# Kernel tuning notes

Hardware: AMD Instinct MI355X
Metric: run time of the kernel (lower is better)

The kernel has to match this reference:

```python
import jax, jax.numpy as jnp
import numpy as np

B, N, K = 2, 8192, 16
D_IN, D_OUT = 32, 128
EPS = 1e-5


def _bn(x, gamma, beta):
    # x: (B, C, L); BatchNorm1d training-mode stats over (B, L)
    mean = x.mean(axis=(0, 2), keepdims=True)
    var = x.var(axis=(0, 2), keepdims=True)
    return gamma[None, :, None] * (x - mean) * jax.lax.rsqrt(var + EPS) + beta[None, :, None]


def _shared_mlp(x, w, b, gamma, beta, act):
    # SharedMLP: 1x1 Conv1d (channel GEMM) + BN + activation. x: (B, Cin, L)
    y = jnp.einsum('oi,bil->bol', w, x) + b[None, :, None]
    return act(_bn(y, gamma, beta))


def _attentive_pool(x, w, b):
    # x: (B, C, N, K); per-(b,n,k) Linear over C, softmax over K, weighted sum over K
    scores = jnp.einsum('oc,bcnk->bonk', w, x) + b[None, :, None, None]
    scores = jax.nn.softmax(scores, axis=-1)
    return jnp.sum(scores * x, axis=-1)  # (B, C, N)  (torch keeps K=1 dim; squeezed by SharedMLP reshape)


def _knn(coords, k):
    # brute-force squared-L2 KNN excluding self (faiss IndexFlatL2 semantics)
    sq = jnp.sum(coords * coords, axis=-1)  # (B, N)
    d2 = sq[:, :, None] + sq[:, None, :] - 2.0 * jnp.einsum('bid,bjd->bij', coords, coords)
    n = coords.shape[1]
    d2 = jnp.where(jnp.eye(n, dtype=bool)[None], jnp.inf, d2)
    neg, idx = jax.lax.top_k(-d2, k)  # ascending squared distance
    return idx, jnp.maximum(-neg, 0.0)


def _lse(coords, features, idx, dist, w, b, gamma, beta):
    # LocalSpatialEncoding: gather neighbor coords, build 10-ch relative features, MLP, concat
    Bq, Nq, Kq = idx.shape
    neighbor = jax.vmap(lambda c, i: c[i])(coords, idx)  # (B, N, K, 3)
    center = jnp.broadcast_to(coords[:, :, None, :], neighbor.shape)
    rel = center - neighbor
    spatial = jnp.concatenate([center, neighbor, rel, dist[..., None]], axis=-1)  # (B, N, K, 10)
    spatial = spatial.transpose(0, 3, 1, 2).reshape(Bq, 10, Nq * Kq)
    sf = _shared_mlp(spatial, w, b, gamma, beta, jax.nn.relu).reshape(Bq, -1, Nq, Kq)
    feat = jnp.broadcast_to(features[..., None], (Bq, features.shape[1], Nq, Kq))
    return jnp.concatenate([sf, feat], axis=1)


def _forward(coords, features,
             mlp1_w, mlp1_b, mlp1_g, mlp1_bt,
             lse1_w, lse1_b, lse1_g, lse1_bt,
             mlpp1_w, mlpp1_b, mlpp1_g, mlpp1_bt,
             lse2_w, lse2_b, lse2_g, lse2_bt,
             mlp2_w, mlp2_b, mlp2_g, mlp2_bt,
             res_w, res_b, res_g, res_bt,
             pool1_w, pool1_b, pool2_w, pool2_b):
    # faiss output is detached in torch (numpy round-trip) -> stop_gradient
    idx, dist = _knn(jax.lax.stop_gradient(coords), K)
    lrelu02 = lambda v: jnp.where(v >= 0, v, 0.2 * v)   # LeakyReLU(0.2)
    lrelu01 = lambda v: jnp.where(v >= 0, v, 0.01 * v)  # default LeakyReLU
    x = _shared_mlp(features, mlp1_w, mlp1_b, mlp1_g, mlp1_bt, lrelu02)      # (B, 64, N)
    x = _lse(coords, x, idx, dist, lse1_w, lse1_b, lse1_g, lse1_bt)          # (B, 128, N, K)
    x = _attentive_pool(x, pool1_w, pool1_b)                                  # (B, 128, N)
    x = _shared_mlp(x, mlpp1_w, mlpp1_b, mlpp1_g, mlpp1_bt, jax.nn.relu)     # (B, 32, N)
    x = _lse(coords, x, idx, dist, lse2_w, lse2_b, lse2_g, lse2_bt)          # (B, 64, N, K)
    x = _attentive_pool(x, pool2_w, pool2_b)                                  # (B, 64, N)
    x_main = _shared_mlp(x, mlp2_w, mlp2_b, mlp2_g, mlp2_bt, jax.nn.relu)    # (B, 128, N)
    resid = _shared_mlp(features, res_w, res_b, res_g, res_bt, jax.nn.relu)  # (B, 128, N)
    return lrelu01(jnp.concatenate([x_main, resid], axis=1))                 # (B, 256, N)


def setup_inputs() -> dict:
    key = jax.random.key(0)
    ks = iter(jax.random.split(key, 64))

    def lin(ci, co):
        w = jax.random.normal(next(ks), (co, ci), jnp.float32) / np.float32(np.sqrt(ci))
        b = jax.random.normal(next(ks), (co,), jnp.float32) * 0.01
        return w, b

    inp = {}
    inp['coords'] = jax.random.normal(next(ks), (B, N, 3), jnp.float32)
    inp['features'] = jax.random.normal(next(ks), (B, D_IN, N), jnp.float32)
    for name, ci, co in [('mlp1', D_IN, D_OUT // 2), ('lse1', 10, D_OUT // 2),
                         ('mlpp1', D_OUT, D_OUT // 4), ('lse2', 10, D_OUT // 4),
                         ('mlp2', D_OUT // 2, D_OUT), ('res', D_IN, D_OUT)]:
        w, b = lin(ci, co)
        inp[name + '_w'], inp[name + '_b'] = w, b
        inp[name + '_g'] = jnp.ones((co,), jnp.float32)
        inp[name + '_bt'] = jnp.zeros((co,), jnp.float32)
    for name, c in [('pool1', D_OUT), ('pool2', D_OUT // 2)]:
        w, b = lin(c, c)
        inp[name + '_w'], inp[name + '_b'] = w, b
    return inp


def reference(coords, features,
              mlp1_w, mlp1_b, mlp1_g, mlp1_bt,
              lse1_w, lse1_b, lse1_g, lse1_bt,
              mlpp1_w, mlpp1_b, mlpp1_g, mlpp1_bt,
              lse2_w, lse2_b, lse2_g, lse2_bt,
              mlp2_w, mlp2_b, mlp2_g, mlp2_bt,
              res_w, res_b, res_g, res_bt,
              pool1_w, pool1_b, pool2_w, pool2_b):
    return _forward(coords, features,
                    mlp1_w, mlp1_b, mlp1_g, mlp1_bt,
                    lse1_w, lse1_b, lse1_g, lse1_bt,
                    mlpp1_w, mlpp1_b, mlpp1_g, mlpp1_bt,
                    lse2_w, lse2_b, lse2_g, lse2_bt,
                    mlp2_w, mlp2_b, mlp2_g, mlp2_bt,
                    res_w, res_b, res_g, res_bt,
                    pool1_w, pool1_b, pool2_w, pool2_b)
```

## Files before the change

kernel.cpp:

```cpp
#include <hip/hip_runtime.h>

static constexpr int N_ = 8192;
static constexpr int B_ = 2;
static constexpr int K_ = 16;

typedef __attribute__((ext_vector_type(8))) short bf16x8;
typedef __attribute__((ext_vector_type(4))) float f32x4;

__device__ __forceinline__ short f2bf(float f) {
  unsigned int u = __float_as_uint(f);
  unsigned int r = (u + 0x7FFFu + ((u >> 16) & 1u)) >> 16;
  return (short)r;
}
__device__ __forceinline__ float bf2f(short h) {
  return __uint_as_float(((unsigned int)(unsigned short)h) << 16);
}
__device__ __forceinline__ float dpp_shr1_f(float x) {
  return __uint_as_float((unsigned int)__builtin_amdgcn_update_dpp(
      0, (int)__float_as_uint(x), 0x111, 0xF, 0xF, true));
}
__device__ __forceinline__ int dpp_shr1_i(int x) {
  return __builtin_amdgcn_update_dpp(0, x, 0x111, 0xF, 0xF, true);
}
__device__ __forceinline__ float rdlane_f(float x, int l) {
  return __uint_as_float(__builtin_amdgcn_readlane(__float_as_uint(x), l));
}

__global__ __launch_bounds__(512) void knn_kernel(const float* __restrict__ coords,
                                                  int* __restrict__ oidx,
                                                  float* __restrict__ odist) {
  __shared__ float4 pts[2048];
  const int b = blockIdx.y;
  const int wv = threadIdx.x >> 6;
  const int lane = threadIdx.x & 63;
  const bool lpos = (lane != 0);
  const int q0 = blockIdx.x * 16 + wv * 2;
  const int q1 = q0 + 1;
  const float* cb = coords + (size_t)b * N_ * 3;
  const float qx0 = cb[q0 * 3 + 0], qy0 = cb[q0 * 3 + 1], qz0 = cb[q0 * 3 + 2];
  const float qx1 = cb[q1 * 3 + 0], qy1 = cb[q1 * 3 + 1], qz1 = cb[q1 * 3 + 2];
  const float qsq0 = fmaf(qx0, qx0, fmaf(qy0, qy0, qz0 * qz0));
  const float qsq1 = fmaf(qx1, qx1, fmaf(qy1, qy1, qz1 * qz1));
  const int qblk0 = q0 & ~63, qblk1 = q1 & ~63;
  const unsigned long long qbit0 = ~(1ull << (q0 & 63));
  const unsigned long long qbit1 = ~(1ull << (q1 & 63));
  float kd0 = INFINITY, kd1 = INFINITY;
  int ki0 = 0, ki1 = 0;
  float tau0 = INFINITY, tau1 = INFINITY;
  for (int t0 = 0; t0 < N_; t0 += 2048) {
    __syncthreads();
    for (int i = threadIdx.x; i < 2048; i += 512) {
      const int p = t0 + i;
      const float x = cb[p * 3 + 0], y = cb[p * 3 + 1], z = cb[p * 3 + 2];
      const float sq = fmaf(x, x, fmaf(y, y, z * z));
      pts[i] = make_float4(x, y, z, sq);
    }
    __syncthreads();
    for (int s = 0; s < 2048; s += 64) {
      const float4 p = pts[s + lane];
      const int base = t0 + s;
      const float dot0 = fmaf(qx0, p.x, fmaf(qy0, p.y, qz0 * p.z));
      const float dot1 = fmaf(qx1, p.x, fmaf(qy1, p.y, qz1 * p.z));
      const float d20 = fmaf(-2.0f, dot0, qsq0 + p.w);
      const float d21 = fmaf(-2.0f, dot1, qsq1 + p.w);
      unsigned long long m0 = __ballot(d20 < tau0);
      unsigned long long m1 = __ballot(d21 < tau1);
      if (base == qblk0) m0 &= qbit0;
      if (base == qblk1) m1 &= qbit1;
      if (m0) {
        do {
          const int src = __builtin_ctzll(m0);
          const float dc = rdlane_f(d20, src);
          const int jc = base + src;
          const float sd = dpp_shr1_f(kd0);
          const int si = dpp_shr1_i(ki0);
          const bool c1 = kd0 > dc;
          const bool c2 = lpos && (sd > dc);
          kd0 = c1 ? (c2 ? sd : dc) : kd0;
          ki0 = c1 ? (c2 ? si : jc) : ki0;
          m0 &= (m0 - 1);
        } while (m0);
        tau0 = rdlane_f(kd0, 15);
      }
      if (m1) {
        do {
          const int src = __builtin_ctzll(m1);
          const float dc = rdlane_f(d21, src);
          const int jc = base + src;
          const float sd = dpp_shr1_f(kd1);
          const int si = dpp_shr1_i(ki1);
          const bool c1 = kd1 > dc;
          const bool c2 = lpos && (sd > dc);
          kd1 = c1 ? (c2 ? sd : dc) : kd1;
          ki1 = c1 ? (c2 ? si : jc) : ki1;
          m1 &= (m1 - 1);
        } while (m1);
        tau1 = rdlane_f(kd1, 15);
      }
    }
  }
  if (lane < 16) {
    oidx[((size_t)b * N_ + q0) * K_ + lane] = ki0;
    odist[((size_t)b * N_ + q0) * K_ + lane] = fmaxf(kd0, 0.0f);
    oidx[((size_t)b * N_ + q1) * K_ + lane] = ki1;
    odist[((size_t)b * N_ + q1) * K_ + lane] = fmaxf(kd1, 0.0f);
  }
}

__device__ __forceinline__ float snn_get(const float* SNN, int a, int b) {
  const int i = a < b ? a : b, j = a < b ? b : a;
  return SNN[i == 0 ? j : (i == 1 ? 2 + j : 3 + j)];
}
__device__ __forceinline__ float mom_mean(int i, const float* C, const float* SN, float Sd) {
  if (i < 3) return 16.0f * C[i];
  if (i < 6) return SN[i - 3];
  if (i < 9) return 16.0f * C[i - 6] - SN[i - 6];
  return Sd;
}
__device__ __forceinline__ float mom_prod(int i, int j, const float* C, const float* SN,
                                          const float* SNN, float Sd, float Sdd, const float* SND) {
  const int ti = i < 3 ? 0 : (i < 6 ? 1 : (i < 9 ? 2 : 3));
  const int tj = j < 3 ? 0 : (j < 6 ? 1 : (j < 9 ? 2 : 3));
  const int a = (ti == 3) ? 0 : (i - ti * 3);
  const int bb = (tj == 3) ? 0 : (j - tj * 3);
  if (ti == 0 && tj == 0) return 16.0f * C[a] * C[bb];
  if (ti == 0 && tj == 1) return C[a] * SN[bb];
  if (ti == 0 && tj == 2) return C[a] * (16.0f * C[bb] - SN[bb]);
  if (ti == 0 && tj == 3) return C[a] * Sd;
  if (ti == 1 && tj == 1) return snn_get(SNN, a, bb);
  if (ti == 1 && tj == 2) return C[bb] * SN[a] - snn_get(SNN, a, bb);
  if (ti == 1 && tj == 3) return SND[a];
  if (ti == 2 && tj == 2) return 16.0f * C[a] * C[bb] - C[a] * SN[bb] - C[bb] * SN[a] + snn_get(SNN, a, bb);
  if (ti == 2 && tj == 3) return C[a] * Sd - SND[a];
  return Sdd;
}

__global__ __launch_bounds__(64) void moments_kernel(const float* __restrict__ coords,
                                                     const int* __restrict__ knn_i,
                                                     const float* __restrict__ knn_d,
                                                     double* __restrict__ mom) {
  const int t = blockIdx.x * 64 + threadIdx.x;
  const int b = t >> 13, n = t & (N_ - 1);
  const float* cb = coords + (size_t)b * N_ * 3;
  float C[3] = {cb[n * 3 + 0], cb[n * 3 + 1], cb[n * 3 + 2]};
  float SN[3] = {0.f, 0.f, 0.f}, SNN[6] = {0.f, 0.f, 0.f, 0.f, 0.f, 0.f};
  float SND[3] = {0.f, 0.f, 0.f}, Sd = 0.f, Sdd = 0.f;
  for (int k = 0; k < K_; ++k) {
    const int id = knn_i[(size_t)t * K_ + k];
    const float dd = knn_d[(size_t)t * K_ + k];
    const float nx = cb[id * 3 + 0], ny = cb[id * 3 + 1], nz = cb[id * 3 + 2];
    SN[0] += nx; SN[1] += ny; SN[2] += nz;
    SNN[0] += nx * nx; SNN[1] += nx * ny; SNN[2] += nx * nz;
    SNN[3] += ny * ny; SNN[4] += ny * nz; SNN[5] += nz * nz;
    Sd += dd; Sdd += dd * dd;
    SND[0] += nx * dd; SND[1] += ny * dd; SND[2] += nz * dd;
  }
  float m65[65];
  int e = 0;
#pragma unroll
  for (int i = 0; i < 10; ++i) m65[e++] = mom_mean(i, C, SN, Sd);
#pragma unroll
  for (int i = 0; i < 10; ++i)
#pragma unroll
    for (int j = i; j < 10; ++j) m65[e++] = mom_prod(i, j, C, SN, SNN, Sd, Sdd, SND);
#pragma unroll
  for (int q = 0; q < 65; ++q) {
    float v = m65[q];
#pragma unroll
    for (int off = 32; off > 0; off >>= 1) v += __shfl_xor(v, off);
    m65[q] = v;
  }
  __shared__ float buf[65];
  if (threadIdx.x == 0) {
#pragma unroll
    for (int q = 0; q < 65; ++q) buf[q] = m65[q];
  }
  __syncthreads();
  if (threadIdx.x < 64) atomicAdd(&mom[threadIdx.x], (double)buf[threadIdx.x]);
  if (threadIdx.x == 0) atomicAdd(&mom[64], (double)buf[64]);
}

template <int CI, int CO>
__device__ __forceinline__ void conv_frag_seg(const float* __restrict__ w, short* __restrict__ H,
                                              short* __restrict__ L, int tid, int nthr) {
  constexpr int NT = CO / 16;
  for (int i = tid; i < CI * CO; i += nthr) {
    const int j = i & 7, l = (i >> 3) & 63, tmp = i >> 9;
    const int tt = tmp % NT, cc = tmp / NT;
    const int c = cc * 32 + (l >> 4) * 8 + j;
    const int o = tt * 16 + (l & 15);
    const float v = w[o * CI + c];
    const short h = f2bf(v);
    H[i] = h;
    L[i] = f2bf(v - bf2f(h));
  }
}

__global__ __launch_bounds__(256) void convert_kernel(
    const float* __restrict__ pw1, const float* __restrict__ pw2,
    short* __restrict__ wB1, short* __restrict__ wB2,
    const float* __restrict__ wm1, short* __restrict__ f1H, short* __restrict__ f1L,
    const float* __restrict__ wmp, short* __restrict__ f2H, short* __restrict__ f2L,
    const float* __restrict__ wm2, short* __restrict__ f3H, short* __restrict__ f3L,
    const float* __restrict__ wrs, short* __restrict__ fRH, short* __restrict__ fRL) {
  const int blk = blockIdx.x;
  if (blk < 8) {
    const int tid = blk * 256 + threadIdx.x;
    for (int i = tid; i < 128 * 128; i += 2048) wB1[i] = f2bf(pw1[i]);
  } else if (blk < 10) {
    const int tid = (blk - 8) * 256 + threadIdx.x;
    for (int i = tid; i < 64 * 64; i += 512) wB2[i] = f2bf(pw2[i]);
  } else if (blk < 12) {
    conv_frag_seg<32, 64>(wm1, f1H, f1L, (blk - 10) * 256 + threadIdx.x, 512);
  } else if (blk < 16) {
    conv_frag_seg<128, 32>(wmp, f2H, f2L, (blk - 12) * 256 + threadIdx.x, 1024);
  } else if (blk < 24) {
    conv_frag_seg<64, 128>(wm2, f3H, f3L, (blk - 16) * 256 + threadIdx.x, 2048);
  } else {
    conv_frag_seg<32, 128>(wrs, fRH, fRL, (blk - 24) * 256 + threadIdx.x, 1024);
  }
}

__global__ void setup_kernel(const double* __restrict__ mom,
                             const float* __restrict__ w1, const float* __restrict__ b1,
                             const float* __restrict__ g1, const float* __restrict__ t1,
                             const float* __restrict__ w2, const float* __restrict__ b2,
                             const float* __restrict__ g2, const float* __restrict__ t2,
                             float* __restrict__ w1f8, float* __restrict__ w2f8) {
  const int t = threadIdx.x;
  __shared__ double mu[10];
  __shared__ double S[10][10];
  const double cnt = (double)B_ * N_ * K_;
  if (t < 10) mu[t] = mom[t] / cnt;
  if (t < 55) {
    int e = t, i = 0;
    while (e >= 10 - i) { e -= 10 - i; ++i; }
    const int j = i + e;
    const double v = mom[10 + t] / cnt;
    S[i][j] = v;
    S[j][i] = v;
  }
  __syncthreads();
  const float *w, *bias, *gg, *bt;
  float *wf;
  int c;
  if (t < 64) { w = w1; bias = b1; gg = g1; bt = t1; wf = w1f8; c = t; }
  else if (t < 96) { w = w2; bias = b2; gg = g2; bt = t2; wf = w2f8; c = t - 64; }
  else return;
  double wd[10];
#pragma unroll
  for (int d = 0; d < 10; ++d) wd[d] = (double)w[c * 10 + d];
  const double cbv = (double)bias[c];
  double mz = cbv;
  for (int d = 0; d < 10; ++d) mz += wd[d] * mu[d];
  double e2 = cbv * cbv;
  for (int d = 0; d < 10; ++d) e2 += 2.0 * cbv * wd[d] * mu[d];
  for (int d = 0; d < 10; ++d)
    for (int e = 0; e < 10; ++e) e2 += wd[d] * wd[e] * S[d][e];
  const double var = e2 - mz * mz;
  const double a = (double)gg[c] / sqrt(var + 1e-5);
  const double shift = (double)bt[c] - a * mz;
  wf[c * 8 + 0] = (float)(a * (wd[0] + wd[6]));
  wf[c * 8 + 1] = (float)(a * (wd[1] + wd[7]));
  wf[c * 8 + 2] = (float)(a * (wd[2] + wd[8]));
  wf[c * 8 + 3] = (float)(a * (wd[3] - wd[6]));
  wf[c * 8 + 4] = (float)(a * (wd[4] - wd[7]));
  wf[c * 8 + 5] = (float)(a * (wd[5] - wd[8]));
  wf[c * 8 + 6] = (float)(a * wd[9]);
  wf[c * 8 + 7] = (float)(a * cbv + shift);
}

template <int CI, int CO, bool ROWMAJ>
__global__ __launch_bounds__(256) void gemm_mfma_kernel(const float* __restrict__ in,
                                                        const short* __restrict__ fragH,
                                                        const short* __restrict__ fragL,
                                                        const float* __restrict__ bias,
                                                        float* __restrict__ out,
                                                        double* __restrict__ sacc) {
  constexpr int NT = CO / 16;
  constexpr int NC = CI / 32;
  __shared__ float part[4][CO][2];
  const int wv = threadIdx.x >> 6, l = threadIdx.x & 63;
  const int col = l & 15, quad = l >> 4;
  const int p0 = blockIdx.x * 64 + wv * 16;
  const int pt = p0 + col;
  f32x4 d[NT];
#pragma unroll
  for (int t = 0; t < NT; ++t) {
    const float bv = bias[t * 16 + col];
    d[t][0] = bv; d[t][1] = bv; d[t][2] = bv; d[t][3] = bv;
  }
#pragma unroll
  for (int cc = 0; cc < NC; ++cc) {
    float xv[8];
    if (ROWMAJ) {
      const float* ip = in + (size_t)pt * CI + cc * 32 + quad * 8;
      *(float4*)&xv[0] = *(const float4*)ip;
      *(float4*)&xv[4] = *(const float4*)(ip + 4);
    } else {
      const int b = pt >> 13, n = pt & (N_ - 1);
      const float* ip = in + ((size_t)b * CI + cc * 32 + quad * 8) * N_ + n;
#pragma unroll
      for (int j = 0; j < 8; ++j) xv[j] = ip[(size_t)j * N_];
    }
    union { bf16x8 v; short u[8]; } AH, AL;
#pragma unroll
    for (int j = 0; j < 8; ++j) {
      const short h = f2bf(xv[j]);
      AH.u[j] = h;
      AL.u[j] = f2bf(xv[j] - bf2f(h));
    }
#pragma unroll
    for (int t = 0; t < NT; ++t) {
      const size_t fo = ((size_t)(cc * NT + t) * 64 + l) * 8;
      const bf16x8 BH = *(const bf16x8*)(fragH + fo);
      const bf16x8 BL = *(const bf16x8*)(fragL + fo);
      d[t] = __builtin_amdgcn_mfma_f32_16x16x32_bf16(AH.v, BH, d[t], 0, 0, 0);
      d[t] = __builtin_amdgcn_mfma_f32_16x16x32_bf16(AH.v, BL, d[t], 0, 0, 0);
      d[t] = __builtin_amdgcn_mfma_f32_16x16x32_bf16(AL.v, BH, d[t], 0, 0, 0);
    }
  }
#pragma unroll
  for (int t = 0; t < NT; ++t) {
#pragma unroll
    for (int r = 0; r < 4; ++r)
      out[(size_t)(p0 + quad * 4 + r) * CO + t * 16 + col] = d[t][r];
    float s1 = d[t][0] + d[t][1] + d[t][2] + d[t][3];
    float s2 = d[t][0] * d[t][0] + d[t][1] * d[t][1] + d[t][2] * d[t][2] + d[t][3] * d[t][3];
    s1 += __shfl_xor(s1, 16); s1 += __shfl_xor(s1, 32);
    s2 += __shfl_xor(s2, 16); s2 += __shfl_xor(s2, 32);
    if (quad == 0) { part[wv][t * 16 + col][0] = s1; part[wv][t * 16 + col][1] = s2; }
  }
  __syncthreads();
  if (threadIdx.x < CO) {
    const int o = threadIdx.x;
    atomicAdd(&sacc[o], (double)(part[0][o][0] + part[1][o][0] + part[2][o][0] + part[3][o][0]));
    atomicAdd(&sacc[CO + o], (double)(part[0][o][1] + part[1][o][1] + part[2][o][1] + part[3][o][1]));
  }
}

template <int CSF, int CF>
__global__ __launch_bounds__(256) void pool_kernel(
    const float* __restrict__ coords, const int* __restrict__ knn_i, const float* __restrict__ knn_d,
    const float* __restrict__ w8,
    const float* __restrict__ feat, const double* __restrict__ sfe,
    const float* __restrict__ gfe, const float* __restrict__ tfe,
    const float slope,
    const short* __restrict__ wB, const float* __restrict__ pb,
    float* __restrict__ out) {
  constexpr int C = CSF + CF;
  constexpr int CP = C + 4;
  constexpr int NT = C / 16;
  constexpr int NC = C / 32;
  __shared__ float xcat[4][16][CP];
  __shared__ float4 sp4[4][16];
  __shared__ float4 spc[4];
  const int g = threadIdx.x >> 6;
  const int l = threadIdx.x & 63;
  const int quad = l >> 4, col = l & 15;
  const int pid = blockIdx.x * 4 + g;
  const int b = pid >> 13, n = pid & (N_ - 1);
  const float* cb = coords + (size_t)b * N_ * 3;

  if (l < 16) {
    const int id = knn_i[(size_t)pid * K_ + l];
    const float dd = knn_d[(size_t)pid * K_ + l];
    const float nx = cb[id * 3 + 0], ny = cb[id * 3 + 1], nz = cb[id * 3 + 2];
    sp4[g][l] = make_float4(nx, ny, nz, dd);
    if (l == 0) spc[g] = make_float4(cb[n * 3 + 0], cb[n * 3 + 1], cb[n * 3 + 2], 0.0f);
  }
  if (l < CF) {
    const double cnt = (double)(B_ * N_);
    const double mean = sfe[l] / cnt;
    const double var = sfe[CF + l] / cnt - mean * mean;
    const double av = (double)gfe[l] / sqrt(var + 1e-5);
    const float af = (float)av;
    const float bfv = (float)((double)tfe[l] - av * mean);
    float v = feat[(size_t)pid * CF + l];
    v = af * v + bfv;
    v = (v >= 0.0f) ? v : slope * v;
#pragma unroll
    for (int j = 0; j < 16; ++j) xcat[g][j][CSF + l] = v;
  }
  __syncthreads();
  if (l < CSF) {
    const float4 wA = *(const float4*)(w8 + l * 8);
    const float4 wBv = *(const float4*)(w8 + l * 8 + 4);
    const float4 C4 = spc[g];
    const float tterm = wBv.w + wA.x * C4.x + wA.y * C4.y + wA.z * C4.z;
#pragma unroll
    for (int k = 0; k < 16; ++k) {
      const float4 nk = sp4[g][k];
      const float z = tterm + wA.w * nk.x + wBv.x * nk.y + wBv.y * nk.z + wBv.z * nk.w;
      xcat[g][k][l] = fmaxf(z, 0.0f);
    }
  }
  __syncthreads();
  f32x4 d[NT];
#pragma unroll
  for (int t = 0; t < NT; ++t) {
    const float pbv = pb[t * 16 + col];
    d[t][0] = pbv; d[t][1] = pbv; d[t][2] = pbv; d[t][3] = pbv;
  }
#pragma unroll
  for (int cc = 0; cc < NC; ++cc) {
    const float* xr = &xcat[g][col][cc * 32 + quad * 8];
    const float4 xa = *(const float4*)xr;
    const float4 xb = *(const float4*)(xr + 4);
    union { bf16x8 v; short u[8]; } A;
    A.u[0] = f2bf(xa.x); A.u[1] = f2bf(xa.y); A.u[2] = f2bf(xa.z); A.u[3] = f2bf(xa.w);
    A.u[4] = f2bf(xb.x); A.u[5] = f2bf(xb.y); A.u[6] = f2bf(xb.z); A.u[7] = f2bf(xb.w);
#pragma unroll
    for (int t = 0; t < NT; ++t) {
      const bf16x8 Bv = *(const bf16x8*)(wB + (size_t)(t * 16 + col) * C + cc * 32 + quad * 8);
      d[t] = __builtin_amdgcn_mfma_f32_16x16x32_bf16(A.v, Bv, d[t], 0, 0, 0);
    }
  }
#pragma unroll
  for (int t = 0; t < NT; ++t) {
    float mx = fmaxf(fmaxf(d[t][0], d[t][1]), fmaxf(d[t][2], d[t][3]));
    mx = fmaxf(mx, __shfl_xor(mx, 16));
    mx = fmaxf(mx, __shfl_xor(mx, 32));
    float e0 = __expf(d[t][0] - mx), e1 = __expf(d[t][1] - mx);
    float e2 = __expf(d[t][2] - mx), e3 = __expf(d[t][3] - mx);
    float s = e0 + e1 + e2 + e3;
    s += __shfl_xor(s, 16);
    s += __shfl_xor(s, 32);
    const int o = t * 16 + col;
    float part = e0 * xcat[g][quad * 4 + 0][o] + e1 * xcat[g][quad * 4 + 1][o] +
                 e2 * xcat[g][quad * 4 + 2][o] + e3 * xcat[g][quad * 4 + 3][o];
    part += __shfl_xor(part, 16);
    part += __shfl_xor(part, 32);
    if (quad == 0) out[(size_t)pid * C + o] = part / s;
  }
}

__global__ __launch_bounds__(256) void final_kernel(const float* __restrict__ y3,
                                                    const float* __restrict__ yr,
                                                    const double* __restrict__ s3,
                                                    const float* __restrict__ g3, const float* __restrict__ t3,
                                                    const double* __restrict__ sr,
                                                    const float* __restrict__ gr, const float* __restrict__ tr,
                                                    float* __restrict__ out) {
  __shared__ float tile[256 * 17];
  const int blk = blockIdx.x;
  const int b = blk >> 9;
  const int n0 = (blk & 511) << 4;
  const int c = threadIdx.x;
  const float* src;
  const double* sa;
  const float *gp, *tp;
  int cc;
  if (c < 128) { src = y3; sa = s3; gp = g3; tp = t3; cc = c; }
  else { src = yr; sa = sr; gp = gr; tp = tr; cc = c - 128; }
  const double cnt = (double)(B_ * N_);
  const double mean = sa[cc] / cnt;
  const double var = sa[128 + cc] / cnt - mean * mean;
  const double avd = (double)gp[cc] / sqrt(var + 1e-5);
  const float av = (float)avd;
  const float bv = (float)((double)tp[cc] - avd * mean);
#pragma unroll
  for (int nl = 0; nl < 16; ++nl) {
    const float x = av * src[((size_t)(b * N_ + n0 + nl)) * 128 + cc] + bv;
    tile[c * 17 + nl] = fmaxf(x, 0.0f);
  }
  __syncthreads();
  const int np = c & 15, grp = c >> 4;
#pragma unroll
  for (int j = 0; j < 16; ++j) {
    const int c2 = grp * 16 + j;
    out[((size_t)(b * 256 + c2)) * N_ + n0 + np] = tile[c2 * 17 + np];
  }
}

extern "C" void kernel_launch(void* const* d_in, const int* in_sizes, int n_in,
                              void* d_out, int out_size, void* d_ws, size_t ws_size,
                              hipStream_t stream) {
  (void)in_sizes; (void)n_in; (void)out_size; (void)ws_size;
  const float* coords   = (const float*)d_in[0];
  const float* features = (const float*)d_in[1];
  const float* mlp1_w = (const float*)d_in[2];
  const float* mlp1_b = (const float*)d_in[3];
  const float* mlp1_g = (const float*)d_in[4];
  const float* mlp1_t = (const float*)d_in[5];
  const float* lse1_w = (const float*)d_in[6];
  const float* lse1_b = (const float*)d_in[7];
  const float* lse1_g = (const float*)d_in[8];
  const float* lse1_t = (const float*)d_in[9];
  const float* mlpp1_w = (const float*)d_in[10];
  const float* mlpp1_b = (const float*)d_in[11];
  const float* mlpp1_g = (const float*)d_in[12];
  const float* mlpp1_t = (const float*)d_in[13];
  const float* lse2_w = (const float*)d_in[14];
  const float* lse2_b = (const float*)d_in[15];
  const float* lse2_g = (const float*)d_in[16];
  const float* lse2_t = (const float*)d_in[17];
  const float* mlp2_w = (const float*)d_in[18];
  const float* mlp2_b = (const float*)d_in[19];
  const float* mlp2_g = (const float*)d_in[20];
  const float* mlp2_t = (const float*)d_in[21];
  const float* res_w = (const float*)d_in[22];
  const float* res_b = (const float*)d_in[23];
  const float* res_g = (const float*)d_in[24];
  const float* res_t = (const float*)d_in[25];
  const float* pool1_w = (const float*)d_in[26];
  const float* pool1_b = (const float*)d_in[27];
  const float* pool2_w = (const float*)d_in[28];
  const float* pool2_b = (const float*)d_in[29];

  float* wsf = (float*)d_ws;
  int* knn_i = (int*)d_ws;
  float* knn_d = wsf + 262144;
  float* y1 = wsf + 524288;
  float* pooled1 = wsf + 1572864;
  float* y2 = wsf + 3670016;
  float* pooled2 = wsf + 4194304;
  float* y3 = wsf + 5242880;
  float* yr = wsf + 7340032;
  double* dacc = (double*)(wsf + 9437184);
  double* mom = dacc;
  double* sacc_mlp1 = dacc + 65;
  double* sacc_mlpp1 = dacc + 193;
  double* sacc_mlp2 = dacc + 257;
  double* sacc_res = dacc + 513;
  float* fpar = wsf + 9437184 + 1600;
  float* w1f8 = fpar;
  float* w2f8 = w1f8 + 512;
  short* wB1 = (short*)(w2f8 + 256);
  short* wB2 = wB1 + 16384;
  short* f1H = wB2 + 4096;
  short* f1L = f1H + 2048;
  short* f2H = f1L + 2048;
  short* f2L = f2H + 4096;
  short* f3H = f2L + 4096;
  short* f3L = f3H + 8192;
  short* fRH = f3L + 8192;
  short* fRL = fRH + 4096;

  hipMemsetAsync(dacc, 0, 769 * sizeof(double), stream);
  knn_kernel<<<dim3(N_ / 16, B_), 512, 0, stream>>>(coords, knn_i, knn_d);
  convert_kernel<<<28, 256, 0, stream>>>(pool1_w, pool2_w, wB1, wB2,
                                         mlp1_w, f1H, f1L, mlpp1_w, f2H, f2L,
                                         mlp2_w, f3H, f3L, res_w, fRH, fRL);
  moments_kernel<<<256, 64, 0, stream>>>(coords, knn_i, knn_d, mom);
  setup_kernel<<<1, 128, 0, stream>>>(mom, lse1_w, lse1_b, lse1_g, lse1_t,
                                      lse2_w, lse2_b, lse2_g, lse2_t, w1f8, w2f8);
  gemm_mfma_kernel<32, 64, false><<<256, 256, 0, stream>>>(features, f1H, f1L, mlp1_b, y1, sacc_mlp1);
  pool_kernel<64, 64><<<B_ * N_ / 4, 256, 0, stream>>>(
      coords, knn_i, knn_d, w1f8, y1, sacc_mlp1, mlp1_g, mlp1_t, 0.2f, wB1, pool1_b, pooled1);
  gemm_mfma_kernel<128, 32, true><<<256, 256, 0, stream>>>(pooled1, f2H, f2L, mlpp1_b, y2, sacc_mlpp1);
  pool_kernel<32, 32><<<B_ * N_ / 4, 256, 0, stream>>>(
      coords, knn_i, knn_d, w2f8, y2, sacc_mlpp1, mlpp1_g, mlpp1_t, 0.0f, wB2, pool2_b, pooled2);
  gemm_mfma_kernel<64, 128, true><<<256, 256, 0, stream>>>(pooled2, f3H, f3L, mlp2_b, y3, sacc_mlp2);
  gemm_mfma_kernel<32, 128, false><<<256, 256, 0, stream>>>(features, fRH, fRL, res_b, yr, sacc_res);
  final_kernel<<<B_ * 512, 256, 0, stream>>>(y3, yr, sacc_mlp2, mlp2_g, mlp2_t,
                                             sacc_res, res_g, res_t, (float*)d_out);
}
```

Measured before the change: 422.7 us.

## Process one query per wavefront in KNN kernel with smaller blocks

The KNN kernel now gives each wavefront one query point instead of two. Blocks shrink to 256 threads and the shared-memory tile to 1024 points, and the grid grows to N/4 blocks per batch. This doubles the number of waves and removes the serialized second insertion loop per wave, so more waves can run and hide latency. The cost is that each loaded point tile is reused by fewer queries, so global loads and LDS fills double.

```diff
diff --git a/kernel.cpp b/kernel.cpp
--- a/kernel.cpp
+++ b/kernel.cpp
@@ -26,84 +26,59 @@
   return __uint_as_float(__builtin_amdgcn_readlane(__float_as_uint(x), l));
 }
 
-__global__ __launch_bounds__(512) void knn_kernel(const float* __restrict__ coords,
+__global__ __launch_bounds__(256) void knn_kernel(const float* __restrict__ coords,
                                                   int* __restrict__ oidx,
                                                   float* __restrict__ odist) {
-  __shared__ float4 pts[2048];
+  __shared__ float4 pts[1024];
   const int b = blockIdx.y;
   const int wv = threadIdx.x >> 6;
   const int lane = threadIdx.x & 63;
   const bool lpos = (lane != 0);
-  const int q0 = blockIdx.x * 16 + wv * 2;
-  const int q1 = q0 + 1;
+  const int q = blockIdx.x * 4 + wv;
   const float* cb = coords + (size_t)b * N_ * 3;
-  const float qx0 = cb[q0 * 3 + 0], qy0 = cb[q0 * 3 + 1], qz0 = cb[q0 * 3 + 2];
-  const float qx1 = cb[q1 * 3 + 0], qy1 = cb[q1 * 3 + 1], qz1 = cb[q1 * 3 + 2];
-  const float qsq0 = fmaf(qx0, qx0, fmaf(qy0, qy0, qz0 * qz0));
-  const float qsq1 = fmaf(qx1, qx1, fmaf(qy1, qy1, qz1 * qz1));
-  const int qblk0 = q0 & ~63, qblk1 = q1 & ~63;
-  const unsigned long long qbit0 = ~(1ull << (q0 & 63));
-  const unsigned long long qbit1 = ~(1ull << (q1 & 63));
-  float kd0 = INFINITY, kd1 = INFINITY;
-  int ki0 = 0, ki1 = 0;
-  float tau0 = INFINITY, tau1 = INFINITY;
-  for (int t0 = 0; t0 < N_; t0 += 2048) {
+  const float qx = cb[q * 3 + 0], qy = cb[q * 3 + 1], qz = cb[q * 3 + 2];
+  const float qsq = fmaf(qx, qx, fmaf(qy, qy, qz * qz));
+  const int qblk = q & ~63;
+  const unsigned long long qbit = ~(1ull << (q & 63));
+  float kd = INFINITY;
+  int ki = 0;
+  float tau = INFINITY;
+  for (int t0 = 0; t0 < N_; t0 += 1024) {
     __syncthreads();
-    for (int i = threadIdx.x; i < 2048; i += 512) {
+    for (int i = threadIdx.x; i < 1024; i += 256) {
       const int p = t0 + i;
       const float x = cb[p * 3 + 0], y = cb[p * 3 + 1], z = cb[p * 3 + 2];
       const float sq = fmaf(x, x, fmaf(y, y, z * z));
       pts[i] = make_float4(x, y, z, sq);
     }
     __syncthreads();
-    for (int s = 0; s < 2048; s += 64) {
+    for (int s = 0; s < 1024; s += 64) {
       const float4 p = pts[s + lane];
       const int base = t0 + s;
-      const float dot0 = fmaf(qx0, p.x, fmaf(qy0, p.y, qz0 * p.z));
-      const float dot1 = fmaf(qx1, p.x, fmaf(qy1, p.y, qz1 * p.z));
-      const float d20 = fmaf(-2.0f, dot0, qsq0 + p.w);
-      const float d21 = fmaf(-2.0f, dot1, qsq1 + p.w);
-      unsigned long long m0 = __ballot(d20 < tau0);
-      unsigned long long m1 = __ballot(d21 < tau1);
-      if (base == qblk0) m0 &= qbit0;
-      if (base == qblk1) m1 &= qbit1;
-      if (m0) {
+      const float dot = fmaf(qx, p.x, fmaf(qy, p.y, qz * p.z));
+      const float d2 = fmaf(-2.0f, dot, qsq + p.w);
+      unsigned long long m = __ballot(d2 < tau);
+      if (base == qblk) m &= qbit;
+      if (m) {
         do {
-          const int src = __builtin_ctzll(m0);
-          const float dc = rdlane_f(d20, src);
+          const int src = __builtin_ctzll(m);
+          const float dc = rdlane_f(d2, src);
           const int jc = base + src;
-          const float sd = dpp_shr1_f(kd0);
-          const int si = dpp_shr1_i(ki0);
-          const bool c1 = kd0 > dc;
+          const float sd = dpp_shr1_f(kd);
+          const int si = dpp_shr1_i(ki);
+          const bool c1 = kd > dc;
           const bool c2 = lpos && (sd > dc);
-          kd0 = c1 ? (c2 ? sd : dc) : kd0;
-          ki0 = c1 ? (c2 ? si : jc) : ki0;
-          m0 &= (m0 - 1);
-        } while (m0);
-        tau0 = rdlane_f(kd0, 15);
+          kd = c1 ? (c2 ? sd : dc) : kd;
+          ki = c1 ? (c2 ? si : jc) : ki;
+          m &= (m - 1);
+        } while (m);
+        tau = rdlane_f(kd, 15);
       }
-      if (m1) {
-        do {
-          const int src = __builtin_ctzll(m1);
-          const float dc = rdlane_f(d21, src);
-          const int jc = base + src;
-          const float sd = dpp_shr1_f(kd1);
-          const int si = dpp_shr1_i(ki1);
-          const bool c1 = kd1 > dc;
-          const bool c2 = lpos && (sd > dc);
-          kd1 = c1 ? (c2 ? sd : dc) : kd1;
-          ki1 = c1 ? (c2 ? si : jc) : ki1;
-          m1 &= (m1 - 1);
-        } while (m1);
-        tau1 = rdlane_f(kd1, 15);
-      }
     }
   }
   if (lane < 16) {
-    oidx[((size_t)b * N_ + q0) * K_ + lane] = ki0;
-    odist[((size_t)b * N_ + q0) * K_ + lane] = fmaxf(kd0, 0.0f);
-    oidx[((size_t)b * N_ + q1) * K_ + lane] = ki1;
-    odist[((size_t)b * N_ + q1) * K_ + lane] = fmaxf(kd1, 0.0f);
+    oidx[((size_t)b * N_ + q) * K_ + lane] = ki;
+    odist[((size_t)b * N_ + q) * K_ + lane] = fmaxf(kd, 0.0f);
   }
 }
 
@@ -538,7 +513,7 @@
   short* fRL = fRH + 4096;
 
   hipMemsetAsync(dacc, 0, 769 * sizeof(double), stream);
-  knn_kernel<<<dim3(N_ / 16, B_), 512, 0, stream>>>(coords, knn_i, knn_d);
+  knn_kernel<<<dim3(N_ / 4, B_), 256, 0, stream>>>(coords, knn_i, knn_d);
   convert_kernel<<<28, 256, 0, stream>>>(pool1_w, pool2_w, wB1, wB2,
                                          mlp1_w, f1H, f1L, mlpp1_w, f2H, f2L,
                                          mlp2_w, f3H, f3L, res_w, fRH, fRL);
```

Result: no change. 423.5 us (+0.2%).
